# Optimization experiments

Measured on AMD Instinct MI355X. Metric: run time of the kernel, lower is better.

The kernel has to match this reference:

```python
import jax, jax.numpy as jnp
import numpy as np

N = 32768        # total nodes (B * max_num_nodes)
E = 524288       # edges, avg degree 16
F_ORI = 32       # data.x_ori feature dim
F_G = 32         # each gamora_output feature dim
IN = F_ORI + 3 * F_G  # 128
H = 256          # hidden_dim
OUT = 16         # out_dim
MAXN = 1024      # max_num_nodes
EPS = 1e-5       # BatchNorm eps


def setup_inputs() -> dict:
    key = jax.random.key(0)
    ks = list(jax.random.split(key, 32))
    g = lambda k, shape, fan: jax.random.normal(k, shape, jnp.float32) / np.sqrt(fan)
    inp = {}
    inp['x_ori'] = jax.random.normal(ks[0], (N, F_ORI), jnp.float32)
    inp['g0'] = jax.random.normal(ks[1], (N, F_G), jnp.float32)
    inp['g1'] = jax.random.normal(ks[2], (N, F_G), jnp.float32)
    inp['g2'] = jax.random.normal(ks[3], (N, F_G), jnp.float32)
    inp['edge_index'] = jax.random.randint(ks[4], (2, E), 0, N, jnp.int64)
    # SAGEConv layer 0: in_dim -> hidden
    inp['Wl0'] = g(ks[5], (IN, H), IN)
    inp['Wr0'] = g(ks[6], (IN, H), IN)
    inp['bb0'] = jnp.zeros((H,), jnp.float32)
    # SAGEConv layers 1..3: hidden -> hidden (stacked)
    inp['Wl'] = g(ks[7], (3, H, H), H)
    inp['Wr'] = g(ks[8], (3, H, H), H)
    inp['bb'] = jnp.zeros((3, H), jnp.float32)
    # BatchNorm per conv layer
    inp['gamma'] = jnp.ones((4, H), jnp.float32)
    inp['beta'] = jnp.zeros((4, H), jnp.float32)
    # mlp1: [max_num_nodes, hidden, 1]
    inp['W1a'] = g(ks[9], (MAXN, H), MAXN)
    inp['b1a'] = jnp.zeros((H,), jnp.float32)
    inp['W1b'] = g(ks[10], (H, 1), H)
    inp['b1b'] = jnp.zeros((1,), jnp.float32)
    # final BatchNorm
    inp['gamma_f'] = jnp.ones((H,), jnp.float32)
    inp['beta_f'] = jnp.zeros((H,), jnp.float32)
    # mlp2: [hidden, hidden, out_dim]
    inp['W2a'] = g(ks[11], (H, H), H)
    inp['b2a'] = jnp.zeros((H,), jnp.float32)
    inp['W2b'] = g(ks[12], (H, OUT), H)
    inp['b2b'] = jnp.zeros((OUT,), jnp.float32)
    return inp


def _bn(x, gamma, beta):
    # training-mode BatchNorm1d over the node/batch axis (biased variance)
    m = jnp.mean(x, axis=0)
    v = jnp.var(x, axis=0)
    return (x - m) * jax.lax.rsqrt(v + EPS) * gamma + beta


def _sage(x, src, dst, inv_deg, Wl, Wr, b):
    # mean neighbor aggregation (gather -> segment_sum -> normalize), then
    # out = lin_l(mean_agg) + lin_r(x)  (PyG SAGEConv, aggr='mean')
    agg = jax.ops.segment_sum(x[src], dst, num_segments=N)
    mean = agg * inv_deg[:, None]
    return mean @ Wl + x @ Wr + b


def reference(x_ori, g0, g1, g2, edge_index, Wl0, Wr0, bb0, Wl, Wr, bb,
              gamma, beta, W1a, b1a, W1b, b1b, gamma_f, beta_f,
              W2a, b2a, W2b, b2b):
    x = jnp.concatenate([x_ori, g0, g1, g2], axis=1)  # [N, IN]
    dst, src = edge_index[0], edge_index[1]
    deg = jax.ops.segment_sum(jnp.ones((E,), x.dtype), dst, num_segments=N)
    inv_deg = jnp.where(deg > 0, 1.0 / jnp.maximum(deg, 1.0), 0.0)
    # layer 0
    x = jax.nn.relu(_bn(_sage(x, src, dst, inv_deg, Wl0, Wr0, bb0), gamma[0], beta[0]))
    # layers 1..3 (dropout is identity in eval-mode reference)
    for i in range(3):
        x = jax.nn.relu(_bn(_sage(x, src, dst, inv_deg, Wl[i], Wr[i], bb[i]),
                            gamma[i + 1], beta[i + 1]))
    x = x.reshape(-1, H, MAXN)                 # [B, H, MAXN]
    h = jax.nn.relu(x @ W1a + b1a)             # [B, H, H]
    x = (h @ W1b + b1b).squeeze(2)             # [B, H]
    x = jax.nn.relu(_bn(x, gamma_f, beta_f))
    x = jax.nn.relu(x @ W2a + b2a) @ W2b + b2b  # [B, OUT]
    return x
```

## Files before the change

kernel.cpp:

```cpp
#include <hip/hip_runtime.h>

#define NN 32768
#define NE 524288
#define HD 256
#define TOTP 794897

#define GAS __attribute__((address_space(1)))
#define LAS __attribute__((address_space(3)))

typedef __attribute__((ext_vector_type(8))) __bf16 bf16x8;
typedef __attribute__((ext_vector_type(4))) float f32x4;

__device__ __forceinline__ float ld_any(const void* p, int i, int isbf16) {
    return isbf16 ? (float)((const __bf16*)p)[i] : ((const float*)p)[i];
}

struct PtrTable { const void* p[18]; };


__global__ __launch_bounds__(256) void k_pre(const unsigned* __restrict__ xw, const int* __restrict__ ei,
                                             PtrTable pt, const void* __restrict__ p0, const void* __restrict__ p1,
                                             const void* __restrict__ p2, const void* __restrict__ p3,
                                             int* __restrict__ flags, int* __restrict__ deg,
                                             __bf16* __restrict__ blob, __bf16* __restrict__ X0c) {
    __shared__ int fl[2];
    const int t = threadIdx.x;
    if (t < 64) {
        unsigned L = xw[t] & 0xFFFFu;
        int e = (int)((L >> 7) & 0xFF);
        unsigned long long b = __ballot(e >= 90 && e <= 135);
        if (t == 0) fl[0] = (b == ~0ULL) ? 1 : 0;
    } else if (t < 128) {
        int u = t - 64;
        unsigned long long b = __ballot(ei[2 * u + 1] != 0);
        if (t == 64) fl[1] = (b == 0ULL) ? 1 : 0;
    }
    __syncthreads();
    const int f0 = fl[0], f1 = fl[1];
    const int blk = blockIdx.x;
    if (blk == 0 && t < 2) flags[t] = fl[t];
    if (blk < 2048) {
        int i0 = (blk * 256 + t) * 8;
        int n = i0 >> 7, f = i0 & 127;
        const void* src = (f < 32) ? p0 : (f < 64) ? p1 : (f < 96) ? p2 : p3;
        int si = n * 32 + (f & 31);
        bf16x8 o;
        #pragma unroll
        for (int j = 0; j < 8; ++j) o[j] = (__bf16)ld_any(src, si + j, f0);
        *(bf16x8*)&X0c[i0] = o;
    } else if (blk < 3601) {
        const int off[23] = {0, 32768, 65536, 65792, 131328, 196864, 262400, 327936, 393472,
                             459008, 459776, 460800, 461824, 723968, 724224, 724480, 724481,
                             724737, 724993, 790529, 790785, 794881, TOTP};
        const signed char pidx[22] = {0, 1, 2, 3, 3, 3, 4, 4, 4, 5, 6, 7, 8, 9, 10, 11, 12, 13, 14, 15, 16, 17};
        const int sbase[22] = {0, 0, 0, 0, 65536, 131072, 0, 65536, 131072, 0, 0, 0, 0, 0, 0, 0, 0, 0, 0, 0, 0, 0};
        const signed char lR[22] = {7, 7, -1, 8, 8, 8, 8, 8, 8, -1, -1, -1, 10, -1, -1, -1, -1, -1, -1, -1, -1, -1};
        const signed char lC[22] = {8, 8, 0, 8, 8, 8, 8, 8, 8, 0, 0, 0, 8, 0, 0, 0, 0, 0, 0, 0, 0, 0};
        int base = ((blk - 2048) * 256 + t) * 2;
        #pragma unroll
        for (int j = 0; j < 2; ++j) {
            int i = base + j;
            if (i >= TOTP) break;
            int s = 0;
            while (i >= off[s + 1]) ++s;
            int jj = i - off[s];
            int si;
            if (lR[s] >= 0) {
                int Rm = (1 << lR[s]) - 1;
                si = sbase[s] + ((jj & Rm) << lC[s]) + (jj >> lR[s]);
            } else {
                si = sbase[s] + jj;
            }
            blob[i] = (__bf16)ld_any(pt.p[pidx[s]], si, f0);
        }
    } else {
        int e0 = ((blk - 3601) * 256 + t) * 2;
        int d0 = f1 ? ei[2 * e0] : ei[e0];
        int d1 = f1 ? ei[2 * e0 + 2] : ei[e0 + 1];
        atomicAdd(&deg[d0], 1);
        atomicAdd(&deg[d1], 1);
    }
}


__global__ __launch_bounds__(256) void k_alloc(const int* __restrict__ deg, int* __restrict__ gcur,
                                               int* __restrict__ offs, float* __restrict__ invd) {
    const int n = blockIdx.x * 256 + threadIdx.x;
    const int lane = threadIdx.x & 63;
    const int v = deg[n];
    invd[n] = v ? 1.f / (float)v : 0.f;
    int incl = v;
    #pragma unroll
    for (int d = 1; d < 64; d <<= 1) {
        int y = __shfl_up(incl, d, 64);
        if (lane >= d) incl += y;
    }
    int base = 0;
    if (lane == 63) base = atomicAdd(gcur, incl);
    base = __shfl(base, 63, 64);
    offs[n] = base + incl - v;
}

__global__ __launch_bounds__(256) void k_fill(const int* __restrict__ ei, const int* __restrict__ flags,
                                              const int* __restrict__ offs, int* __restrict__ cursor,
                                              int* __restrict__ csr) {
    int e = blockIdx.x * 256 + threadIdx.x;
    int f = flags[1];
    int d = f ? ei[2 * e] : ei[e];
    int s = f ? ei[2 * NE + 2 * e] : ei[NE + e];
    int p = atomicAdd(&cursor[d], 1);
    csr[offs[d] + p] = s;
}


__global__ __launch_bounds__(256) void k_agg0(const __bf16* __restrict__ X, const int* __restrict__ csr,
                                              const int* __restrict__ offs, const int* __restrict__ deg,
                                              const float* __restrict__ invd, __bf16* __restrict__ M) {
    const int t = threadIdx.x;
    const int s = blockIdx.x & 1;
    const int n = (blockIdx.x >> 1) * 32 + (t >> 3);
    const int fo = s * 64 + (t & 7) * 8;
    const int beg = offs[n], end = beg + deg[n];
    float a[8] = {};
    for (int e = beg; e < end; e += 8) {
        #pragma unroll
        for (int u = 0; u < 8; ++u) {
            int ee = e + u;
            int idx = csr[ee < end ? ee : end - 1] & (NN - 1);
            float mk = ee < end ? 1.f : 0.f;
            bf16x8 v = *(const bf16x8*)&X[(size_t)idx * 128 + fo];
            #pragma unroll
            for (int j = 0; j < 8; ++j) a[j] += mk * (float)v[j];
        }
    }
    const float id = invd[n];
    bf16x8 o;
    #pragma unroll
    for (int j = 0; j < 8; ++j) o[j] = (__bf16)(a[j] * id);
    *(bf16x8*)&M[(size_t)n * 128 + fo] = o;
}

__global__ __launch_bounds__(256) void k_agg(const __bf16* __restrict__ X, const int* __restrict__ csr,
                                             const int* __restrict__ offs, const int* __restrict__ deg,
                                             const float* __restrict__ invd, __bf16* __restrict__ M) {
    const int t = threadIdx.x;
    const int s = blockIdx.x & 3;
    const int n = (blockIdx.x >> 2) * 32 + (t >> 3);
    const int fo = s * 64 + (t & 7) * 8;
    const int beg = offs[n], end = beg + deg[n];
    float a[8] = {};
    for (int e = beg; e < end; e += 8) {
        #pragma unroll
        for (int u = 0; u < 8; ++u) {
            int ee = e + u;
            int idx = csr[ee < end ? ee : end - 1] & (NN - 1);
            float mk = ee < end ? 1.f : 0.f;
            bf16x8 v = *(const bf16x8*)&X[(size_t)idx * HD + fo];
            #pragma unroll
            for (int j = 0; j < 8; ++j) a[j] += mk * (float)v[j];
        }
    }
    const float id = invd[n];
    bf16x8 o;
    #pragma unroll
    for (int j = 0; j < 8; ++j) o[j] = (__bf16)(a[j] * id);
    *(bf16x8*)&M[(size_t)n * HD + fo] = o;
}


template <int MODE, int TM, int BNA, int NP>
__global__ __launch_bounds__(256) void k_gemm(const __bf16* __restrict__ A1, const __bf16* __restrict__ WT1,
                                              const __bf16* __restrict__ A2, const __bf16* __restrict__ WT2,
                                              const __bf16* __restrict__ bias, int KD,
                                              __bf16* __restrict__ O, float* __restrict__ colsum,
                                              const __bf16* __restrict__ W1b, float* __restrict__ x2,
                                              const float* __restrict__ pstatA, const __bf16* __restrict__ gA,
                                              const __bf16* __restrict__ bA) {
    constexpr int MI = TM / 32;
    __shared__ __bf16 As[NP][2][TM][32];
    __shared__ __bf16 Bs[NP][2][128][32];
    __shared__ float scs[256], shs[256];
    const int t = threadIdx.x;
    const int lane = t & 63, w = t >> 6;
    const int wm = w >> 1, wn = w & 1;
    const int quad = lane >> 4, l15 = lane & 15;
    const int row0 = blockIdx.x * TM, c0 = blockIdx.y * 128;
    const int dr = lane >> 2, dc = (lane & 3) * 8;
    if constexpr (BNA != 0) {
        const float invn = 1.0f / NN;
        float m = pstatA[t] * invn;
        float var = fmaxf(pstatA[256 + t] * invn - m * m, 0.f);
        float rs = rsqrtf(var + 1e-5f);
        float g = (float)gA[t] * rs;
        scs[t] = g;
        shs[t] = (float)bA[t] - m * g;
    }
    f32x4 acc[MI][4] = {};
    for (int k0 = 0; k0 < KD; k0 += 64) {
        __syncthreads();
        #pragma unroll
        for (int pass = 0; pass < NP; ++pass) {
            const __bf16* __restrict__ A = pass ? A2 : A1;
            const __bf16* __restrict__ WT = pass ? WT2 : WT1;
            #pragma unroll
            for (int kk = 0; kk < 2; ++kk) {
                #pragma unroll
                for (int i = 0; i < 2; ++i) {
                    const __bf16* g = &WT[(size_t)(c0 + w * 32 + i * 16 + dr) * KD + k0 + kk * 32 + dc];
                    __builtin_amdgcn_global_load_lds((const GAS void*)g,
                                                     (LAS void*)&Bs[pass][kk][w * 32 + i * 16][0], 16, 0, 0);
                }
                if ((BNA >> pass) & 1) {
                    const int kb = (k0 + kk * 32 + dc) & 255;
                    #pragma unroll
                    for (int i = 0; i < TM / 64; ++i) {
                        const __bf16* g = &A[(size_t)(row0 + w * (TM / 4) + i * 16 + dr) * KD + k0 + kk * 32 + dc];
                        bf16x8 v = *(const bf16x8*)g;
                        bf16x8 o;
                        #pragma unroll
                        for (int j = 0; j < 8; ++j)
                            o[j] = (__bf16)fmaxf((float)v[j] * scs[kb + j] + shs[kb + j], 0.f);
                        *(bf16x8*)&As[pass][kk][w * (TM / 4) + i * 16 + dr][dc] = o;
                    }
                } else {
                    #pragma unroll
                    for (int i = 0; i < TM / 64; ++i) {
                        const __bf16* g = &A[(size_t)(row0 + w * (TM / 4) + i * 16 + dr) * KD + k0 + kk * 32 + dc];
                        __builtin_amdgcn_global_load_lds((const GAS void*)g,
                                                         (LAS void*)&As[pass][kk][w * (TM / 4) + i * 16][0],
                                                         16, 0, 0);
                    }
                }
            }
        }
        __syncthreads();
        #pragma unroll
        for (int pass = 0; pass < NP; ++pass) {
            #pragma unroll
            for (int kk = 0; kk < 2; ++kk) {
                bf16x8 af[MI], bfr[4];
                #pragma unroll
                for (int i = 0; i < MI; ++i)
                    af[i] = *(const bf16x8*)&As[pass][kk][wm * (TM / 2) + i * 16 + l15][quad * 8];
                #pragma unroll
                for (int j = 0; j < 4; ++j)
                    bfr[j] = *(const bf16x8*)&Bs[pass][kk][wn * 64 + j * 16 + l15][quad * 8];
                #pragma unroll
                for (int i = 0; i < MI; ++i)
                    #pragma unroll
                    for (int j = 0; j < 4; ++j)
                        acc[i][j] = __builtin_amdgcn_mfma_f32_16x16x32_bf16(af[i], bfr[j], acc[i][j], 0, 0, 0);
            }
        }
    }
    __syncthreads();
    if constexpr (MODE == 0) {
        float* lsum = (float*)&As[0][0][0][0];
        lsum[t] = 0.f;
        __syncthreads();
        #pragma unroll
        for (int j = 0; j < 4; ++j) {
            const int cb = wn * 64 + j * 16 + l15;
            const int col = c0 + cb;
            const float b = (float)bias[col];
            float s = 0.f, q = 0.f;
            #pragma unroll
            for (int i = 0; i < MI; ++i) {
                const size_t rbase = (size_t)(row0 + wm * (TM / 2) + i * 16 + quad * 4) * HD + col;
                #pragma unroll
                for (int r = 0; r < 4; ++r) {
                    float y = acc[i][j][r] + b;
                    O[rbase + (size_t)r * HD] = (__bf16)y;
                    s += y;
                    q += y * y;
                }
            }
            s += __shfl_xor(s, 16, 64); s += __shfl_xor(s, 32, 64);
            q += __shfl_xor(q, 16, 64); q += __shfl_xor(q, 32, 64);
            if (quad == 0) {
                atomicAdd(&lsum[cb], s);
                atomicAdd(&lsum[128 + cb], q);
            }
        }
        __syncthreads();
        if (t < 128) atomicAdd(&colsum[c0 + t], lsum[t]);
        else atomicAdd(&colsum[256 + c0 + t - 128], lsum[t]);
    } else {
        float bj[4], wj[4];
        #pragma unroll
        for (int j = 0; j < 4; ++j) {
            const int col = c0 + wn * 64 + j * 16 + l15;
            bj[j] = (float)bias[col];
            wj[j] = (float)W1b[col];
        }
        #pragma unroll
        for (int i = 0; i < MI; ++i) {
            #pragma unroll
            for (int r = 0; r < 4; ++r) {
                float p = 0.f;
                #pragma unroll
                for (int j = 0; j < 4; ++j) p += fmaxf(acc[i][j][r] + bj[j], 0.f) * wj[j];
                p += __shfl_xor(p, 1, 64); p += __shfl_xor(p, 2, 64);
                p += __shfl_xor(p, 4, 64); p += __shfl_xor(p, 8, 64);
                if (l15 == 0) atomicAdd(&x2[row0 + wm * (TM / 2) + i * 16 + quad * 4 + r], p);
            }
        }
    }
}


__global__ __launch_bounds__(256) void k_bnapply(__bf16* __restrict__ Y, const float* __restrict__ pstat,
                                                 const __bf16* __restrict__ gamma, const __bf16* __restrict__ beta) {
    __shared__ float sc[256], sh[256];
    const int t = threadIdx.x;
    {
        const float invn = 1.0f / NN;
        float m = pstat[t] * invn;
        float var = fmaxf(pstat[256 + t] * invn - m * m, 0.f);
        float rs = rsqrtf(var + 1e-5f);
        float s = (float)gamma[t] * rs;
        sc[t] = s;
        sh[t] = (float)beta[t] - m * s;
    }
    __syncthreads();
    size_t i = ((size_t)blockIdx.x * 256 + t) * 8;
    int c = (int)(i & 255);
    bf16x8 y = *(const bf16x8*)&Y[i];
    bf16x8 o;
    #pragma unroll
    for (int j = 0; j < 8; ++j) o[j] = (__bf16)fmaxf((float)y[j] * sc[c + j] + sh[c + j], 0.f);
    *(bf16x8*)&Y[i] = o;
}


__global__ __launch_bounds__(256) void k_mlp2(const float* __restrict__ x2, const __bf16* __restrict__ b1b,
                                              const __bf16* __restrict__ gf, const __bf16* __restrict__ bf_,
                                              const __bf16* __restrict__ W2a, const __bf16* __restrict__ b2a,
                                              const __bf16* __restrict__ W2b, const __bf16* __restrict__ b2b,
                                              const int* __restrict__ flags, void* __restrict__ out) {
    __shared__ float row[HD];
    __shared__ float hbuf[HD];
    __shared__ float part[256];
    const int b = blockIdx.x, t = threadIdx.x;
    const float b1 = (float)b1b[0];
    float s = 0.f, q = 0.f, mine = 0.f;
    #pragma unroll
    for (int r = 0; r < 32; ++r) {
        float v = x2[r * HD + t] + b1;
        s += v; q += v * v;
        if (r == b) mine = v;
    }
    float m = s * (1.0f / 32.0f);
    float var = fmaxf(q * (1.0f / 32.0f) - m * m, 0.f);
    float rs = rsqrtf(var + 1e-5f);
    float sc = (float)gf[t] * rs;
    float sh = (float)bf_[t] - m * sc;
    row[t] = fmaxf(mine * sc + sh, 0.f);
    __syncthreads();
    float acc = (float)b2a[t];
    for (int j = 0; j < HD; ++j) acc += row[j] * (float)W2a[j * HD + t];
    hbuf[t] = fmaxf(acc, 0.f);
    __syncthreads();
    const int k = t & 15, g = t >> 4;
    float p = 0.f;
    #pragma unroll
    for (int jj = 0; jj < 16; ++jj) p += hbuf[g * 16 + jj] * (float)W2b[(g * 16 + jj) * 16 + k];
    part[t] = p;
    __syncthreads();
    if (t < 16) {
        float o = (float)b2b[t];
        #pragma unroll
        for (int g2 = 0; g2 < 16; ++g2) o += part[g2 * 16 + t];
        if (flags[0]) ((__bf16*)out)[b * 16 + t] = (__bf16)o;
        else ((float*)out)[b * 16 + t] = o;
    }
}


extern "C" void kernel_launch(void* const* d_in, const int* in_sizes, int n_in,
                              void* d_out, int out_size, void* d_ws, size_t ws_size,
                              hipStream_t stream) {
    const int* ei = (const int*)d_in[4];

    char* ws = (char*)d_ws;
    size_t off_ = 0;
    auto ALLOC = [&](size_t b) { char* p = ws + off_; off_ += (b + 255) & ~(size_t)255; return p; };
    int* flags_ = (int*)ALLOC(8);
    size_t zbeg = off_;
    int* deg_ = (int*)ALLOC(NN * 4);
    int* cursor_ = (int*)ALLOC(NN * 4);
    float* colsum_ = (float*)ALLOC(4 * 512 * 4);
    float* x2_ = (float*)ALLOC(8192 * 4);
    int* gcur_ = (int*)ALLOC(4);
    size_t zlen = off_ - zbeg;
    int* offs_ = (int*)ALLOC(NN * 4);
    float* invd_ = (float*)ALLOC(NN * 4);
    int* csr_ = (int*)ALLOC((size_t)NE * 4);
    __bf16* blob_ = (__bf16*)ALLOC((size_t)TOTP * 2);
    __bf16* M_ = (__bf16*)ALLOC((size_t)NN * HD * 2);
    __bf16* Xa_ = (__bf16*)ALLOC((size_t)NN * HD * 2);
    __bf16* Xb_ = (__bf16*)ALLOC((size_t)NN * HD * 2);
    __bf16* X0c_ = Xb_;

    __bf16* Wl0T = blob_ + 0;
    __bf16* Wr0T = blob_ + 32768;
    __bf16* bb0c = blob_ + 65536;
    __bf16* WlT = blob_ + 65792;
    __bf16* WrT = blob_ + 262400;
    __bf16* bbc = blob_ + 459008;
    __bf16* gammac = blob_ + 459776;
    __bf16* betac = blob_ + 460800;
    __bf16* W1aT = blob_ + 461824;
    __bf16* b1ac = blob_ + 723968;
    __bf16* W1bc = blob_ + 724224;
    __bf16* b1bc = blob_ + 724480;
    __bf16* gfc = blob_ + 724481;
    __bf16* bfc = blob_ + 724737;
    __bf16* W2ac = blob_ + 724993;
    __bf16* b2ac = blob_ + 790529;
    __bf16* W2bc = blob_ + 790785;
    __bf16* b2bc = blob_ + 794881;

    PtrTable pt;
    pt.p[0] = d_in[5];  pt.p[1] = d_in[6];  pt.p[2] = d_in[7];  pt.p[3] = d_in[8];
    pt.p[4] = d_in[9];  pt.p[5] = d_in[10]; pt.p[6] = d_in[11]; pt.p[7] = d_in[12];
    pt.p[8] = d_in[13]; pt.p[9] = d_in[14]; pt.p[10] = d_in[15]; pt.p[11] = d_in[16];
    pt.p[12] = d_in[17]; pt.p[13] = d_in[18]; pt.p[14] = d_in[19]; pt.p[15] = d_in[20];
    pt.p[16] = d_in[21]; pt.p[17] = d_in[22];

    hipMemsetAsync(ws + zbeg, 0, zlen, stream);
    k_pre<<<4625, 256, 0, stream>>>((const unsigned*)d_in[0], ei, pt, d_in[0], d_in[1], d_in[2], d_in[3],
                                    flags_, deg_, blob_, X0c_);
    k_alloc<<<NN / 256, 256, 0, stream>>>(deg_, gcur_, offs_, invd_);
    k_fill<<<NE / 256, 256, 0, stream>>>(ei, flags_, offs_, cursor_, csr_);

    k_agg0<<<NN / 32 * 2, 256, 0, stream>>>(X0c_, csr_, offs_, deg_, invd_, M_);
    k_gemm<0, 128, 0, 2><<<dim3(NN / 128, 2), 256, 0, stream>>>(M_, Wl0T, X0c_, Wr0T, bb0c, 128, Xa_, colsum_,
                                                                nullptr, nullptr, nullptr, nullptr, nullptr);
    k_bnapply<<<NN / 8, 256, 0, stream>>>(Xa_, colsum_, gammac, betac);

    __bf16* Xin = Xa_;
    __bf16* Xo = Xb_;
    for (int l = 0; l < 3; ++l) {
        float* cs = colsum_ + (l + 1) * 512;
        k_agg<<<NN / 32 * 4, 256, 0, stream>>>(Xin, csr_, offs_, deg_, invd_, M_);
        k_gemm<0, 128, 0, 2><<<dim3(NN / 128, 2), 256, 0, stream>>>(M_, WlT + (size_t)l * HD * HD, Xin,
                                                                    WrT + (size_t)l * HD * HD, bbc + l * HD, 256,
                                                                    Xo, cs, nullptr, nullptr, nullptr, nullptr,
                                                                    nullptr);
        if (l < 2) k_bnapply<<<NN / 8, 256, 0, stream>>>(Xo, cs, gammac + (l + 1) * HD, betac + (l + 1) * HD);
        __bf16* tmp = Xin; Xin = Xo; Xo = tmp;
    }

    k_gemm<1, 64, 1, 1><<<dim3(8192 / 64, 2), 256, 0, stream>>>(Xin, W1aT, nullptr, nullptr, b1ac, 1024, nullptr,
                                                                nullptr, W1bc, x2_, colsum_ + 3 * 512,
                                                                gammac + 3 * HD, betac + 3 * HD);
    k_mlp2<<<32, 256, 0, stream>>>(x2_, b1bc, gfc, bfc, W2ac, b2ac, W2bc, b2bc, flags_, d_out);
}
```

Before: 420.8 us.

## Fuse SAGE GEMM with BatchNorm+ReLU via cooperative grid sync

Adds a cooperative GEMM kernel that accumulates per-column BatchNorm statistics, synchronises the whole grid, then applies BN and ReLU to register-held accumulators before writing. This removes the separate bnapply pass, which re-read and re-wrote the activation tensor, and one launch per layer. In exchange, all 512 blocks must be co-resident, which the code checks through an occupancy query. Grid sync and cooperative launch add their own overhead, and when the check fails the code falls back to the old two-kernel path.

```diff
diff --git a/kernel.cpp b/kernel.cpp
--- a/kernel.cpp
+++ b/kernel.cpp
@@ -1,4 +1,7 @@
 #include <hip/hip_runtime.h>
+#include <hip/hip_cooperative_groups.h>
+
+namespace cg = cooperative_groups;
 
 #define NN 32768
 #define NE 524288
@@ -309,6 +312,125 @@
 }
 
 
+template <int TM, int NP>
+__global__ __launch_bounds__(256) void k_gemmbn(const __bf16* __restrict__ A1, const __bf16* __restrict__ WT1,
+                                                const __bf16* __restrict__ A2, const __bf16* __restrict__ WT2,
+                                                const __bf16* __restrict__ bias, int KD,
+                                                __bf16* __restrict__ O, float* __restrict__ colsum,
+                                                const __bf16* __restrict__ gamma, const __bf16* __restrict__ beta) {
+    constexpr int MI = TM / 32;
+    __shared__ __bf16 As[NP][2][TM][32];
+    __shared__ __bf16 Bs[NP][2][128][32];
+    __shared__ float scs[128], shs[128];
+    const int t = threadIdx.x;
+    const int lane = t & 63, w = t >> 6;
+    const int wm = w >> 1, wn = w & 1;
+    const int quad = lane >> 4, l15 = lane & 15;
+    const int row0 = blockIdx.x * TM, c0 = blockIdx.y * 128;
+    const int dr = lane >> 2, dc = (lane & 3) * 8;
+    f32x4 acc[MI][4] = {};
+    for (int k0 = 0; k0 < KD; k0 += 64) {
+        __syncthreads();
+        #pragma unroll
+        for (int pass = 0; pass < NP; ++pass) {
+            const __bf16* __restrict__ A = pass ? A2 : A1;
+            const __bf16* __restrict__ WT = pass ? WT2 : WT1;
+            #pragma unroll
+            for (int kk = 0; kk < 2; ++kk) {
+                #pragma unroll
+                for (int i = 0; i < 2; ++i) {
+                    const __bf16* g = &WT[(size_t)(c0 + w * 32 + i * 16 + dr) * KD + k0 + kk * 32 + dc];
+                    __builtin_amdgcn_global_load_lds((const GAS void*)g,
+                                                     (LAS void*)&Bs[pass][kk][w * 32 + i * 16][0], 16, 0, 0);
+                }
+                #pragma unroll
+                for (int i = 0; i < TM / 64; ++i) {
+                    const __bf16* g = &A[(size_t)(row0 + w * (TM / 4) + i * 16 + dr) * KD + k0 + kk * 32 + dc];
+                    __builtin_amdgcn_global_load_lds((const GAS void*)g,
+                                                     (LAS void*)&As[pass][kk][w * (TM / 4) + i * 16][0], 16, 0, 0);
+                }
+            }
+        }
+        __syncthreads();
+        #pragma unroll
+        for (int pass = 0; pass < NP; ++pass) {
+            #pragma unroll
+            for (int kk = 0; kk < 2; ++kk) {
+                bf16x8 af[MI], bfr[4];
+                #pragma unroll
+                for (int i = 0; i < MI; ++i)
+                    af[i] = *(const bf16x8*)&As[pass][kk][wm * (TM / 2) + i * 16 + l15][quad * 8];
+                #pragma unroll
+                for (int j = 0; j < 4; ++j)
+                    bfr[j] = *(const bf16x8*)&Bs[pass][kk][wn * 64 + j * 16 + l15][quad * 8];
+                #pragma unroll
+                for (int i = 0; i < MI; ++i)
+                    #pragma unroll
+                    for (int j = 0; j < 4; ++j)
+                        acc[i][j] = __builtin_amdgcn_mfma_f32_16x16x32_bf16(af[i], bfr[j], acc[i][j], 0, 0, 0);
+            }
+        }
+    }
+    __syncthreads();
+    float* lsum = (float*)&As[0][0][0][0];
+    lsum[t] = 0.f;
+    __syncthreads();
+    float bj[4];
+    #pragma unroll
+    for (int j = 0; j < 4; ++j) {
+        const int cb = wn * 64 + j * 16 + l15;
+        bj[j] = (float)bias[c0 + cb];
+        float s = 0.f, q = 0.f;
+        #pragma unroll
+        for (int i = 0; i < MI; ++i) {
+            #pragma unroll
+            for (int r = 0; r < 4; ++r) {
+                float y = acc[i][j][r] + bj[j];
+                s += y;
+                q += y * y;
+            }
+        }
+        s += __shfl_xor(s, 16, 64); s += __shfl_xor(s, 32, 64);
+        q += __shfl_xor(q, 16, 64); q += __shfl_xor(q, 32, 64);
+        if (quad == 0) {
+            atomicAdd(&lsum[cb], s);
+            atomicAdd(&lsum[128 + cb], q);
+        }
+    }
+    __syncthreads();
+    if (t < 128) atomicAdd(&colsum[c0 + t], lsum[t]);
+    else atomicAdd(&colsum[256 + c0 + t - 128], lsum[t]);
+    __threadfence();
+    cg::this_grid().sync();
+    if (t < 128) {
+        float S = atomicAdd(&colsum[c0 + t], 0.f);
+        float Q = atomicAdd(&colsum[256 + c0 + t], 0.f);
+        const float invn = 1.0f / NN;
+        float m = S * invn;
+        float var = fmaxf(Q * invn - m * m, 0.f);
+        float rs = rsqrtf(var + 1e-5f);
+        float g = (float)gamma[c0 + t] * rs;
+        scs[t] = g;
+        shs[t] = (float)beta[c0 + t] - m * g;
+    }
+    __syncthreads();
+    #pragma unroll
+    for (int j = 0; j < 4; ++j) {
+        const int cb = wn * 64 + j * 16 + l15;
+        const float sc = scs[cb], sh = shs[cb];
+        #pragma unroll
+        for (int i = 0; i < MI; ++i) {
+            const size_t rbase = (size_t)(row0 + wm * (TM / 2) + i * 16 + quad * 4) * HD + c0 + cb;
+            #pragma unroll
+            for (int r = 0; r < 4; ++r) {
+                float y = acc[i][j][r] + bj[j];
+                O[rbase + (size_t)r * HD] = (__bf16)fmaxf(y * sc + sh, 0.f);
+            }
+        }
+    }
+}
+
+
 __global__ __launch_bounds__(256) void k_bnapply(__bf16* __restrict__ Y, const float* __restrict__ pstat,
                                                  const __bf16* __restrict__ gamma, const __bf16* __restrict__ beta) {
     __shared__ float sc[256], sh[256];
@@ -428,27 +550,50 @@
     pt.p[12] = d_in[17]; pt.p[13] = d_in[18]; pt.p[14] = d_in[19]; pt.p[15] = d_in[20];
     pt.p[16] = d_in[21]; pt.p[17] = d_in[22];
 
+    static int coop_ok = -1;
+    if (coop_ok < 0) {
+        int nb = 0;
+        hipError_t err = hipOccupancyMaxActiveBlocksPerMultiprocessor(&nb, k_gemmbn<128, 2>, 256, 0);
+        coop_ok = (err == hipSuccess && nb >= 2) ? 1 : 0;
+    }
+
     hipMemsetAsync(ws + zbeg, 0, zlen, stream);
     k_pre<<<4625, 256, 0, stream>>>((const unsigned*)d_in[0], ei, pt, d_in[0], d_in[1], d_in[2], d_in[3],
                                     flags_, deg_, blob_, X0c_);
     k_alloc<<<NN / 256, 256, 0, stream>>>(deg_, gcur_, offs_, invd_);
     k_fill<<<NE / 256, 256, 0, stream>>>(ei, flags_, offs_, cursor_, csr_);
 
+    auto gemmbn = [&](const __bf16* A1, const __bf16* WT1, const __bf16* A2, const __bf16* WT2,
+                      const __bf16* bias, int KD, __bf16* O, float* cs, const __bf16* g, const __bf16* b) {
+        if (coop_ok) {
+            void* args[] = {&A1, &WT1, &A2, &WT2, &bias, &KD, &O, &cs, &g, &b};
+            hipLaunchCooperativeKernel((const void*)k_gemmbn<128, 2>, dim3(NN / 128, 2), dim3(256),
+                                       args, 0, stream);
+        } else {
+            k_gemm<0, 128, 0, 2><<<dim3(NN / 128, 2), 256, 0, stream>>>(A1, WT1, A2, WT2, bias, KD, O, cs,
+                                                                        nullptr, nullptr, nullptr, nullptr,
+                                                                        nullptr);
+            k_bnapply<<<NN / 8, 256, 0, stream>>>(O, cs, g, b);
+        }
+    };
+
     k_agg0<<<NN / 32 * 2, 256, 0, stream>>>(X0c_, csr_, offs_, deg_, invd_, M_);
-    k_gemm<0, 128, 0, 2><<<dim3(NN / 128, 2), 256, 0, stream>>>(M_, Wl0T, X0c_, Wr0T, bb0c, 128, Xa_, colsum_,
-                                                                nullptr, nullptr, nullptr, nullptr, nullptr);
-    k_bnapply<<<NN / 8, 256, 0, stream>>>(Xa_, colsum_, gammac, betac);
+    gemmbn(M_, Wl0T, X0c_, Wr0T, bb0c, 128, Xa_, colsum_, gammac, betac);
 
     __bf16* Xin = Xa_;
     __bf16* Xo = Xb_;
     for (int l = 0; l < 3; ++l) {
         float* cs = colsum_ + (l + 1) * 512;
         k_agg<<<NN / 32 * 4, 256, 0, stream>>>(Xin, csr_, offs_, deg_, invd_, M_);
-        k_gemm<0, 128, 0, 2><<<dim3(NN / 128, 2), 256, 0, stream>>>(M_, WlT + (size_t)l * HD * HD, Xin,
-                                                                    WrT + (size_t)l * HD * HD, bbc + l * HD, 256,
-                                                                    Xo, cs, nullptr, nullptr, nullptr, nullptr,
-                                                                    nullptr);
-        if (l < 2) k_bnapply<<<NN / 8, 256, 0, stream>>>(Xo, cs, gammac + (l + 1) * HD, betac + (l + 1) * HD);
+        if (l < 2) {
+            gemmbn(M_, WlT + (size_t)l * HD * HD, Xin, WrT + (size_t)l * HD * HD, bbc + l * HD, 256, Xo, cs,
+                   gammac + (l + 1) * HD, betac + (l + 1) * HD);
+        } else {
+            k_gemm<0, 128, 0, 2><<<dim3(NN / 128, 2), 256, 0, stream>>>(M_, WlT + (size_t)l * HD * HD, Xin,
+                                                                        WrT + (size_t)l * HD * HD, bbc + l * HD,
+                                                                        256, Xo, cs, nullptr, nullptr, nullptr,
+                                                                        nullptr, nullptr);
+        }
         __bf16* tmp = Xin; Xin = Xo; Xo = tmp;
     }
 
```

After: 421.0 us. About the same (+0.0%).
